# Kernel tuning notes

Hardware: AMD Instinct MI355X
Metric: run time of the kernel (lower is better)

Reference implementation:

```python
import jax, jax.numpy as jnp
import numpy as np

H, I, E, TOPK = 1024, 4096, 8, 2
B, S = 2, 2048


def setup_inputs() -> dict:
    key = jax.random.key(0)
    ks = jax.random.split(key, 6)
    x = jax.random.normal(ks[0], (B, S, H), dtype=jnp.float32)
    expert_indices = jax.random.randint(ks[1], (B, S, TOPK), 0, E)
    expert_weights = jax.random.uniform(ks[2], (B, S, TOPK), dtype=jnp.float32)
    gate_proj = jax.random.normal(ks[3], (E, I, H), dtype=jnp.float32) * 0.02
    up_proj = jax.random.normal(ks[4], (E, I, H), dtype=jnp.float32) * 0.02
    down_proj = jax.random.normal(ks[5], (E, H, I), dtype=jnp.float32) * 0.02
    return {"x": x, "expert_indices": expert_indices, "expert_weights": expert_weights,
            "gate_proj": gate_proj, "up_proj": up_proj, "down_proj": down_proj}


def reference(x, expert_indices, expert_weights, gate_proj, up_proj, down_proj):
    b, s, h = x.shape
    xf = x.reshape(-1, h)                      # [T, H]
    ei = expert_indices.reshape(-1, expert_indices.shape[-1])   # [T, K]
    ew = expert_weights.reshape(-1, expert_weights.shape[-1])   # [T, K]
    n_experts = gate_proj.shape[0]
    out = jnp.zeros_like(xf)
    for e in range(n_experts):
        # combined routing weight of this expert per token (sum over topk slots)
        w_e = jnp.sum(jnp.where(ei == e, ew, 0.0), axis=-1)     # [T]
        g = xf @ gate_proj[e].T                # [T, I]
        u = xf @ up_proj[e].T                  # [T, I]
        inter = jax.nn.silu(g) * u             # fused SiLU*mul
        out = out + w_e[:, None] * (inter @ down_proj[e].T)     # weighted scatter-add
    return out.reshape(b, s, h)
```

## Files before the change

kernel.cpp:

```cpp
#include <hip/hip_runtime.h>
#include <cstdint>
#include <cstddef>

#define H_DIM 1024
#define I_DIM 4096
#define E_NUM 8
#define TOPK  2
#define T_NUM 4096
#define NROWS (T_NUM * TOPK)
#define BK    32

typedef _Float16 half8 __attribute__((ext_vector_type(8)));
typedef float    f32x4 __attribute__((ext_vector_type(4)));

__device__ __forceinline__ void async_copy16(void* lds, const void* g)
{
    __builtin_amdgcn_global_load_lds(
        (__attribute__((address_space(1))) unsigned int*)g,
        (__attribute__((address_space(3))) unsigned int*)lds,
        16 , 0 , 0 );
}

__global__ void cvt_f32_to_f16(const float* __restrict__ s, _Float16* __restrict__ d, int n4)
{
    int i = blockIdx.x * blockDim.x + threadIdx.x;
    if (i >= n4) return;
    float4 v = reinterpret_cast<const float4*>(s)[i];
    union { _Float16 h[4]; unsigned long long u; } o;
    o.h[0] = (_Float16)v.x; o.h[1] = (_Float16)v.y;
    o.h[2] = (_Float16)v.z; o.h[3] = (_Float16)v.w;
    reinterpret_cast<unsigned long long*>(d)[i] = o.u;
}

__global__ void route_count(const int* __restrict__ ei, int* __restrict__ counts)
{
    int s = blockIdx.x * blockDim.x + threadIdx.x;
    if (s < NROWS) atomicAdd(&counts[ei[s]], 1);
}

__global__ void route_scatter(const int* __restrict__ ei, const float* __restrict__ ew,
                              const int* __restrict__ counts, int* __restrict__ offs,
                              int* __restrict__ token_of_row, float* __restrict__ weight_of_row)
{
    __shared__ int cur[E_NUM];
    if (threadIdx.x == 0) {
        int acc = 0;
        for (int e = 0; e < E_NUM; ++e) { offs[e] = acc; cur[e] = acc; acc += counts[e]; }
        offs[E_NUM] = acc;
    }
    __syncthreads();
    for (int s = (int)threadIdx.x; s < NROWS; s += (int)blockDim.x) {
        int e = ei[s];
        int r = atomicAdd(&cur[e], 1);
        token_of_row[r]  = s >> 1;
        weight_of_row[r] = ew[s];
    }
}

__global__ __launch_bounds__(256) void gateup_gemm(
    const _Float16* __restrict__ xh,
    const _Float16* __restrict__ Wg,
    const _Float16* __restrict__ Wu,
    const int*      __restrict__ token_of_row,
    const int*      __restrict__ offs,
    _Float16*       __restrict__ inter)
{
    const int e = blockIdx.z;
    const int seg_start = offs[e], seg_end = offs[e + 1];
    const int m0 = seg_start + (int)blockIdx.y * 128;
    if (m0 >= seg_end) return;
    const int n0 = (int)blockIdx.x * 64;

    __shared__ _Float16 Ash[128 * BK];
    __shared__ _Float16 Bgs[64 * BK];
    __shared__ _Float16 Bus[64 * BK];

    const int tid  = (int)threadIdx.x;
    const int lane = tid & 63, wid = tid >> 6;
    const int wm = wid >> 1, wn = wid & 1;

    const int c  = lane & 3;
    const int rl = lane >> 2;

    const _Float16* pA[2];
    _Float16* lA[2];
#pragma unroll
    for (int j = 0; j < 2; ++j) {
        int q = 2 * wid + j;
        int r = m0 + q * 16 + rl;
        if (r > seg_end - 1) r = seg_end - 1;
        int tok = token_of_row[r];
        pA[j] = xh + (size_t)tok * H_DIM + c * 8;
        lA[j] = &Ash[q * 16 * BK];
    }
    const int brow = wid * 16 + rl;
    const _Float16* pBg = Wg + ((size_t)e * I_DIM + n0 + brow) * H_DIM + c * 8;
    const _Float16* pBu = Wu + ((size_t)e * I_DIM + n0 + brow) * H_DIM + c * 8;
    _Float16* lBg = &Bgs[wid * 16 * BK];
    _Float16* lBu = &Bus[wid * 16 * BK];

    f32x4 accg[4][2], accu[4][2];
#pragma unroll
    for (int i = 0; i < 4; ++i)
#pragma unroll
        for (int j = 0; j < 2; ++j) {
            accg[i][j] = (f32x4){0.f, 0.f, 0.f, 0.f};
            accu[i][j] = (f32x4){0.f, 0.f, 0.f, 0.f};
        }

    const int fm = lane & 15, fk = (lane >> 4) * 8;

    for (int kt = 0; kt < H_DIM / BK; ++kt) {
        const int ko = kt * BK;
        __syncthreads();
        async_copy16(lA[0], pA[0] + ko);
        async_copy16(lA[1], pA[1] + ko);
        async_copy16(lBg,   pBg   + ko);
        async_copy16(lBu,   pBu   + ko);
        __syncthreads();

        half8 a[4], bg[2], bu[2];
#pragma unroll
        for (int i = 0; i < 4; ++i)
            a[i] = *(const half8*)&Ash[(wm * 64 + i * 16 + fm) * BK + fk];
#pragma unroll
        for (int j = 0; j < 2; ++j) {
            bg[j] = *(const half8*)&Bgs[(wn * 32 + j * 16 + fm) * BK + fk];
            bu[j] = *(const half8*)&Bus[(wn * 32 + j * 16 + fm) * BK + fk];
        }
#pragma unroll
        for (int i = 0; i < 4; ++i)
#pragma unroll
            for (int j = 0; j < 2; ++j) {
                accg[i][j] = __builtin_amdgcn_mfma_f32_16x16x32_f16(a[i], bg[j], accg[i][j], 0, 0, 0);
                accu[i][j] = __builtin_amdgcn_mfma_f32_16x16x32_f16(a[i], bu[j], accu[i][j], 0, 0, 0);
            }
    }

#pragma unroll
    for (int i = 0; i < 4; ++i) {
#pragma unroll
        for (int reg = 0; reg < 4; ++reg) {
            int r = m0 + wm * 64 + i * 16 + (lane >> 4) * 4 + reg;
            if (r < seg_end) {
#pragma unroll
                for (int j = 0; j < 2; ++j) {
                    int col = n0 + wn * 32 + j * 16 + fm;
                    float g = accg[i][j][reg];
                    float u = accu[i][j][reg];
                    float sv = (g / (1.f + __expf(-g))) * u;
                    inter[(size_t)r * I_DIM + col] = (_Float16)sv;
                }
            }
        }
    }
}

__global__ __launch_bounds__(256) void down_gemm(
    const _Float16* __restrict__ inter,
    const _Float16* __restrict__ Wd,
    const int*      __restrict__ token_of_row,
    const float*    __restrict__ weight_of_row,
    const int*      __restrict__ offs,
    float*          __restrict__ out)
{
    const int e = blockIdx.z;
    const int seg_start = offs[e], seg_end = offs[e + 1];
    const int m0 = seg_start + (int)blockIdx.y * 128;
    if (m0 >= seg_end) return;
    const int n0 = (int)blockIdx.x * 128;

    __shared__ _Float16 Ash[128 * BK];
    __shared__ _Float16 Bsh[128 * BK];

    const int tid  = (int)threadIdx.x;
    const int lane = tid & 63, wid = tid >> 6;
    const int wm = wid >> 1, wn = wid & 1;
    const int c = lane & 3, rl = lane >> 2;

    const _Float16* pA[2]; _Float16* lA[2];
    const _Float16* pB[2]; _Float16* lB[2];
#pragma unroll
    for (int j = 0; j < 2; ++j) {
        int q = 2 * wid + j;
        int row_in = q * 16 + rl;
        int r = m0 + row_in;
        if (r > seg_end - 1) r = seg_end - 1;
        pA[j] = inter + (size_t)r * I_DIM + c * 8;
        lA[j] = &Ash[q * 16 * BK];
        int n = n0 + row_in;
        pB[j] = Wd + ((size_t)e * H_DIM + n) * I_DIM + c * 8;
        lB[j] = &Bsh[q * 16 * BK];
    }

    f32x4 acc[4][4];
#pragma unroll
    for (int i = 0; i < 4; ++i)
#pragma unroll
        for (int j = 0; j < 4; ++j) acc[i][j] = (f32x4){0.f, 0.f, 0.f, 0.f};

    const int fm = lane & 15, fk = (lane >> 4) * 8;

    for (int kt = 0; kt < I_DIM / BK; ++kt) {
        const int ko = kt * BK;
        __syncthreads();
        async_copy16(lA[0], pA[0] + ko);
        async_copy16(lA[1], pA[1] + ko);
        async_copy16(lB[0], pB[0] + ko);
        async_copy16(lB[1], pB[1] + ko);
        __syncthreads();

        half8 a[4], b[4];
#pragma unroll
        for (int i = 0; i < 4; ++i)
            a[i] = *(const half8*)&Ash[(wm * 64 + i * 16 + fm) * BK + fk];
#pragma unroll
        for (int j = 0; j < 4; ++j)
            b[j] = *(const half8*)&Bsh[(wn * 64 + j * 16 + fm) * BK + fk];
#pragma unroll
        for (int i = 0; i < 4; ++i)
#pragma unroll
            for (int j = 0; j < 4; ++j)
                acc[i][j] = __builtin_amdgcn_mfma_f32_16x16x32_f16(a[i], b[j], acc[i][j], 0, 0, 0);
    }

#pragma unroll
    for (int i = 0; i < 4; ++i) {
#pragma unroll
        for (int reg = 0; reg < 4; ++reg) {
            int r = m0 + wm * 64 + i * 16 + (lane >> 4) * 4 + reg;
            if (r < seg_end) {
                float w = weight_of_row[r];
                int   t = token_of_row[r];
#pragma unroll
                for (int j = 0; j < 4; ++j) {
                    int col = n0 + wn * 64 + j * 16 + fm;
                    atomicAdd(&out[(size_t)t * H_DIM + col], w * acc[i][j][reg]);
                }
            }
        }
    }
}

extern "C" void kernel_launch(void* const* d_in, const int* in_sizes, int n_in,
                              void* d_out, int out_size, void* d_ws, size_t ws_size,
                              hipStream_t stream)
{
    const float* x  = (const float*)d_in[0];
    const int*   ei = (const int*)  d_in[1];
    const float* ew = (const float*)d_in[2];
    const float* gp = (const float*)d_in[3];
    const float* up = (const float*)d_in[4];
    const float* dp = (const float*)d_in[5];
    float* out = (float*)d_out;

    char* ws = (char*)d_ws;
    size_t o = 0;
    _Float16* xh    = (_Float16*)(ws + o); o += (size_t)T_NUM * H_DIM * 2;
    _Float16* Wg_h  = (_Float16*)(ws + o); o += (size_t)E_NUM * I_DIM * H_DIM * 2;
    _Float16* Wu_h  = (_Float16*)(ws + o); o += (size_t)E_NUM * I_DIM * H_DIM * 2;
    _Float16* Wd_h  = (_Float16*)(ws + o); o += (size_t)E_NUM * I_DIM * H_DIM * 2;
    _Float16* inter = (_Float16*)(ws + o); o += (size_t)NROWS * I_DIM * 2;
    int*   counts        = (int*)  (ws + o);
    int*   offs          = (int*)  (ws + o + 64);
    int*   token_of_row  = (int*)  (ws + o + 256);
    float* weight_of_row = (float*)(ws + o + 256 + (size_t)NROWS * 4);
    size_t ws_need = o + 256 + (size_t)NROWS * 8;
    if (ws_size < ws_need) return;

    hipMemsetAsync(counts, 0, 64, stream);
    hipMemsetAsync(d_out, 0, (size_t)out_size * sizeof(float), stream);

    const int nt = 256;
    const int nx = T_NUM * H_DIM / 4;
    cvt_f32_to_f16<<<(nx + nt - 1) / nt, nt, 0, stream>>>(x, xh, nx);
    const int nw = E_NUM * I_DIM * H_DIM / 4;
    cvt_f32_to_f16<<<(nw + nt - 1) / nt, nt, 0, stream>>>(gp, Wg_h, nw);
    cvt_f32_to_f16<<<(nw + nt - 1) / nt, nt, 0, stream>>>(up, Wu_h, nw);
    cvt_f32_to_f16<<<(nw + nt - 1) / nt, nt, 0, stream>>>(dp, Wd_h, nw);

    route_count<<<NROWS / 256, 256, 0, stream>>>(ei, counts);
    route_scatter<<<1, 256, 0, stream>>>(ei, ew, counts, offs, token_of_row, weight_of_row);

    gateup_gemm<<<dim3(I_DIM / 64, NROWS / 128, E_NUM), 256, 0, stream>>>(
        xh, Wg_h, Wu_h, token_of_row, offs, inter);
    down_gemm<<<dim3(H_DIM / 128, NROWS / 128, E_NUM), 256, 0, stream>>>(
        inter, Wd_h, token_of_row, weight_of_row, offs, out);
}
```

Before: 773.0 us.

## XOR-swizzle LDS tiles in MoE GEMMs and fuse conversion and routing kernels

Gate-up and down GEMMs now permute which 16-byte K-chunk each lane loads from global memory, using an XOR of the row index. The fragment reads apply the matching XOR so that LDS reads are spread across banks and conflicts are reduced. The four f32-to-f16 conversion launches are merged into one kernel, and the two routing kernels plus a memset are merged into a single-block kernel that counts in shared memory. This removes launch overhead and LDS bank conflicts, but the single-block routing kernel runs serially over all rows.

```diff
diff --git a/kernel.cpp b/kernel.cpp
--- a/kernel.cpp
+++ b/kernel.cpp
@@ -21,35 +21,47 @@
         16 , 0 , 0 );
 }
 
-__global__ void cvt_f32_to_f16(const float* __restrict__ s, _Float16* __restrict__ d, int n4)
+
+#define NX4 (T_NUM * H_DIM / 4)
+#define NW4 (E_NUM * I_DIM * H_DIM / 4)
+__global__ void cvt_all(const float* __restrict__ x,  const float* __restrict__ gp,
+                        const float* __restrict__ up, const float* __restrict__ dp,
+                        _Float16* __restrict__ xh, _Float16* __restrict__ wg,
+                        _Float16* __restrict__ wu, _Float16* __restrict__ wd)
 {
     int i = blockIdx.x * blockDim.x + threadIdx.x;
-    if (i >= n4) return;
-    float4 v = reinterpret_cast<const float4*>(s)[i];
+    const int total = NX4 + 3 * NW4;
+    if (i >= total) return;
+    const float* s; _Float16* d; int j;
+    if (i < NX4)              { s = x;  d = xh; j = i; }
+    else if (i < NX4 + NW4)   { s = gp; d = wg; j = i - NX4; }
+    else if (i < NX4 + 2*NW4) { s = up; d = wu; j = i - NX4 - NW4; }
+    else                      { s = dp; d = wd; j = i - NX4 - 2*NW4; }
+    float4 v = reinterpret_cast<const float4*>(s)[j];
     union { _Float16 h[4]; unsigned long long u; } o;
     o.h[0] = (_Float16)v.x; o.h[1] = (_Float16)v.y;
     o.h[2] = (_Float16)v.z; o.h[3] = (_Float16)v.w;
-    reinterpret_cast<unsigned long long*>(d)[i] = o.u;
-}
-
-__global__ void route_count(const int* __restrict__ ei, int* __restrict__ counts)
-{
-    int s = blockIdx.x * blockDim.x + threadIdx.x;
-    if (s < NROWS) atomicAdd(&counts[ei[s]], 1);
-}
-
-__global__ void route_scatter(const int* __restrict__ ei, const float* __restrict__ ew,
-                              const int* __restrict__ counts, int* __restrict__ offs,
-                              int* __restrict__ token_of_row, float* __restrict__ weight_of_row)
-{
+    reinterpret_cast<unsigned long long*>(d)[j] = o.u;
+}
+
+__global__ void route_all(const int* __restrict__ ei, const float* __restrict__ ew,
+                          int* __restrict__ offs,
+                          int* __restrict__ token_of_row, float* __restrict__ weight_of_row)
+{
+    __shared__ int cnt[E_NUM];
     __shared__ int cur[E_NUM];
-    if (threadIdx.x == 0) {
+    const int t = (int)threadIdx.x;
+    if (t < E_NUM) cnt[t] = 0;
+    __syncthreads();
+    for (int s = t; s < NROWS; s += (int)blockDim.x) atomicAdd(&cnt[ei[s]], 1);
+    __syncthreads();
+    if (t == 0) {
         int acc = 0;
-        for (int e = 0; e < E_NUM; ++e) { offs[e] = acc; cur[e] = acc; acc += counts[e]; }
+        for (int e = 0; e < E_NUM; ++e) { offs[e] = acc; cur[e] = acc; acc += cnt[e]; }
         offs[E_NUM] = acc;
     }
     __syncthreads();
-    for (int s = (int)threadIdx.x; s < NROWS; s += (int)blockDim.x) {
+    for (int s = t; s < NROWS; s += (int)blockDim.x) {
         int e = ei[s];
         int r = atomicAdd(&cur[e], 1);
         token_of_row[r]  = s >> 1;
@@ -79,8 +91,10 @@
     const int lane = tid & 63, wid = tid >> 6;
     const int wm = wid >> 1, wn = wid & 1;
 
-    const int c  = lane & 3;
-    const int rl = lane >> 2;
+    const int c   = lane & 3;
+    const int rl  = lane >> 2;
+    const int frl = (rl & 3) ^ (rl >> 2);
+    const int gc  = c ^ frl;
 
     const _Float16* pA[2];
     _Float16* lA[2];
@@ -90,12 +104,12 @@
         int r = m0 + q * 16 + rl;
         if (r > seg_end - 1) r = seg_end - 1;
         int tok = token_of_row[r];
-        pA[j] = xh + (size_t)tok * H_DIM + c * 8;
+        pA[j] = xh + (size_t)tok * H_DIM + gc * 8;
         lA[j] = &Ash[q * 16 * BK];
     }
     const int brow = wid * 16 + rl;
-    const _Float16* pBg = Wg + ((size_t)e * I_DIM + n0 + brow) * H_DIM + c * 8;
-    const _Float16* pBu = Wu + ((size_t)e * I_DIM + n0 + brow) * H_DIM + c * 8;
+    const _Float16* pBg = Wg + ((size_t)e * I_DIM + n0 + brow) * H_DIM + gc * 8;
+    const _Float16* pBu = Wu + ((size_t)e * I_DIM + n0 + brow) * H_DIM + gc * 8;
     _Float16* lBg = &Bgs[wid * 16 * BK];
     _Float16* lBu = &Bus[wid * 16 * BK];
 
@@ -108,7 +122,9 @@
             accu[i][j] = (f32x4){0.f, 0.f, 0.f, 0.f};
         }
 
-    const int fm = lane & 15, fk = (lane >> 4) * 8;
+    const int fm = lane & 15, kq = lane >> 4;
+    const int fsw = (fm & 3) ^ ((fm >> 2) & 3);
+    const int rdo = (kq ^ fsw) * 8;
 
     for (int kt = 0; kt < H_DIM / BK; ++kt) {
         const int ko = kt * BK;
@@ -122,11 +138,11 @@
         half8 a[4], bg[2], bu[2];
 #pragma unroll
         for (int i = 0; i < 4; ++i)
-            a[i] = *(const half8*)&Ash[(wm * 64 + i * 16 + fm) * BK + fk];
+            a[i] = *(const half8*)&Ash[(wm * 64 + i * 16 + fm) * BK + rdo];
 #pragma unroll
         for (int j = 0; j < 2; ++j) {
-            bg[j] = *(const half8*)&Bgs[(wn * 32 + j * 16 + fm) * BK + fk];
-            bu[j] = *(const half8*)&Bus[(wn * 32 + j * 16 + fm) * BK + fk];
+            bg[j] = *(const half8*)&Bgs[(wn * 32 + j * 16 + fm) * BK + rdo];
+            bu[j] = *(const half8*)&Bus[(wn * 32 + j * 16 + fm) * BK + rdo];
         }
 #pragma unroll
         for (int i = 0; i < 4; ++i)
@@ -141,7 +157,7 @@
     for (int i = 0; i < 4; ++i) {
 #pragma unroll
         for (int reg = 0; reg < 4; ++reg) {
-            int r = m0 + wm * 64 + i * 16 + (lane >> 4) * 4 + reg;
+            int r = m0 + wm * 64 + i * 16 + kq * 4 + reg;
             if (r < seg_end) {
 #pragma unroll
                 for (int j = 0; j < 2; ++j) {
@@ -176,7 +192,10 @@
     const int tid  = (int)threadIdx.x;
     const int lane = tid & 63, wid = tid >> 6;
     const int wm = wid >> 1, wn = wid & 1;
-    const int c = lane & 3, rl = lane >> 2;
+    const int c   = lane & 3;
+    const int rl  = lane >> 2;
+    const int frl = (rl & 3) ^ (rl >> 2);
+    const int gc  = c ^ frl;
 
     const _Float16* pA[2]; _Float16* lA[2];
     const _Float16* pB[2]; _Float16* lB[2];
@@ -186,10 +205,10 @@
         int row_in = q * 16 + rl;
         int r = m0 + row_in;
         if (r > seg_end - 1) r = seg_end - 1;
-        pA[j] = inter + (size_t)r * I_DIM + c * 8;
+        pA[j] = inter + (size_t)r * I_DIM + gc * 8;
         lA[j] = &Ash[q * 16 * BK];
         int n = n0 + row_in;
-        pB[j] = Wd + ((size_t)e * H_DIM + n) * I_DIM + c * 8;
+        pB[j] = Wd + ((size_t)e * H_DIM + n) * I_DIM + gc * 8;
         lB[j] = &Bsh[q * 16 * BK];
     }
 
@@ -199,7 +218,9 @@
 #pragma unroll
         for (int j = 0; j < 4; ++j) acc[i][j] = (f32x4){0.f, 0.f, 0.f, 0.f};
 
-    const int fm = lane & 15, fk = (lane >> 4) * 8;
+    const int fm = lane & 15, kq = lane >> 4;
+    const int fsw = (fm & 3) ^ ((fm >> 2) & 3);
+    const int rdo = (kq ^ fsw) * 8;
 
     for (int kt = 0; kt < I_DIM / BK; ++kt) {
         const int ko = kt * BK;
@@ -213,10 +234,10 @@
         half8 a[4], b[4];
 #pragma unroll
         for (int i = 0; i < 4; ++i)
-            a[i] = *(const half8*)&Ash[(wm * 64 + i * 16 + fm) * BK + fk];
+            a[i] = *(const half8*)&Ash[(wm * 64 + i * 16 + fm) * BK + rdo];
 #pragma unroll
         for (int j = 0; j < 4; ++j)
-            b[j] = *(const half8*)&Bsh[(wn * 64 + j * 16 + fm) * BK + fk];
+            b[j] = *(const half8*)&Bsh[(wn * 64 + j * 16 + fm) * BK + rdo];
 #pragma unroll
         for (int i = 0; i < 4; ++i)
 #pragma unroll
@@ -228,7 +249,7 @@
     for (int i = 0; i < 4; ++i) {
 #pragma unroll
         for (int reg = 0; reg < 4; ++reg) {
-            int r = m0 + wm * 64 + i * 16 + (lane >> 4) * 4 + reg;
+            int r = m0 + wm * 64 + i * 16 + kq * 4 + reg;
             if (r < seg_end) {
                 float w = weight_of_row[r];
                 int   t = token_of_row[r];
@@ -261,26 +282,19 @@
     _Float16* Wu_h  = (_Float16*)(ws + o); o += (size_t)E_NUM * I_DIM * H_DIM * 2;
     _Float16* Wd_h  = (_Float16*)(ws + o); o += (size_t)E_NUM * I_DIM * H_DIM * 2;
     _Float16* inter = (_Float16*)(ws + o); o += (size_t)NROWS * I_DIM * 2;
-    int*   counts        = (int*)  (ws + o);
-    int*   offs          = (int*)  (ws + o + 64);
+    int*   offs          = (int*)  (ws + o);
     int*   token_of_row  = (int*)  (ws + o + 256);
     float* weight_of_row = (float*)(ws + o + 256 + (size_t)NROWS * 4);
     size_t ws_need = o + 256 + (size_t)NROWS * 8;
     if (ws_size < ws_need) return;
 
-    hipMemsetAsync(counts, 0, 64, stream);
     hipMemsetAsync(d_out, 0, (size_t)out_size * sizeof(float), stream);
 
     const int nt = 256;
-    const int nx = T_NUM * H_DIM / 4;
-    cvt_f32_to_f16<<<(nx + nt - 1) / nt, nt, 0, stream>>>(x, xh, nx);
-    const int nw = E_NUM * I_DIM * H_DIM / 4;
-    cvt_f32_to_f16<<<(nw + nt - 1) / nt, nt, 0, stream>>>(gp, Wg_h, nw);
-    cvt_f32_to_f16<<<(nw + nt - 1) / nt, nt, 0, stream>>>(up, Wu_h, nw);
-    cvt_f32_to_f16<<<(nw + nt - 1) / nt, nt, 0, stream>>>(dp, Wd_h, nw);
-
-    route_count<<<NROWS / 256, 256, 0, stream>>>(ei, counts);
-    route_scatter<<<1, 256, 0, stream>>>(ei, ew, counts, offs, token_of_row, weight_of_row);
+    const int ncvt = NX4 + 3 * NW4;
+    cvt_all<<<(ncvt + nt - 1) / nt, nt, 0, stream>>>(x, gp, up, dp, xh, Wg_h, Wu_h, Wd_h);
+
+    route_all<<<1, 1024, 0, stream>>>(ei, ew, offs, token_of_row, weight_of_row);
 
     gateup_gemm<<<dim3(I_DIM / 64, NROWS / 128, E_NUM), 256, 0, stream>>>(
         xh, Wg_h, Wu_h, token_of_row, offs, inter);
```

Result: faster. 713.4 us (-7.7%).
